# Optimization experiments

Measured on AMD Instinct MI355X. Metric: run time of the kernel, lower is better.

Reference implementation:

```python
import jax, jax.numpy as jnp
import numpy as np
from jax import lax

BOS = 1


def setup_inputs() -> dict:
    key = jax.random.key(0)
    ks = jax.random.split(key, 12)
    B, T_ENC, D_ENC = 32, 800, 512   # D_ENC == att_odim
    E, H, V, ATT_H = 256, 512, 10000, 512
    s = 0.02
    return {
        "enc_pad": jax.random.normal(ks[0], (B, T_ENC, D_ENC), jnp.float32),
        "embedding": jax.random.normal(ks[1], (V, E), jnp.float32) * s,
        "W_ih": jax.random.normal(ks[2], (4 * H, E + D_ENC), jnp.float32) * s,
        "W_hh": jax.random.normal(ks[3], (4 * H, H), jnp.float32) * s,
        "b_ih": jnp.zeros((4 * H,), jnp.float32),
        "b_hh": jnp.zeros((4 * H,), jnp.float32),
        "W_enc": jax.random.normal(ks[4], (D_ENC, ATT_H), jnp.float32) * s,
        "W_dec": jax.random.normal(ks[5], (H, ATT_H), jnp.float32) * s,
        "v_att": jax.random.normal(ks[6], (ATT_H,), jnp.float32) * s,
        "W_out": jax.random.normal(ks[7], (V, H + D_ENC), jnp.float32) * s,
        "b_out": jnp.zeros((V,), jnp.float32),
        "enc_len": jax.random.randint(ks[8], (B,), 1, T_ENC + 1).astype(jnp.int32),
        "max_dec_timesteps": 100,
    }


def reference(enc_pad, embedding, W_ih, W_hh, b_ih, b_hh,
              W_enc, W_dec, v_att, W_out, b_out,
              enc_len, max_dec_timesteps):
    B, T, D = enc_pad.shape
    H = W_hh.shape[1]
    mask = jnp.arange(T)[None, :] < enc_len[:, None]          # [B,T]
    enc_proj = jnp.einsum('btd,da->bta', enc_pad, W_enc)       # precomputed enc keys
    NEG = jnp.float32(-1e30)

    def step(carry, _):
        dec_z, dec_c, c, pred = carry
        emb = jnp.take(embedding, pred, axis=0)                # [B,E]
        x = jnp.concatenate([emb, c], axis=-1)                 # cell_inp
        # torch.nn.LSTMCell gates
        gates = x @ W_ih.T + b_ih + dec_z @ W_hh.T + b_hh
        i, f, g, o = jnp.split(gates, 4, axis=-1)
        i, f, o = jax.nn.sigmoid(i), jax.nn.sigmoid(f), jax.nn.sigmoid(o)
        g = jnp.tanh(g)
        dec_c = f * dec_c + i * g
        dec_z = o * jnp.tanh(dec_c)
        # additive attention over encoder frames, masked by enc_len
        e = jnp.tanh(enc_proj + (dec_z @ W_dec)[:, None, :]) @ v_att  # [B,T]
        w = jax.nn.softmax(jnp.where(mask, e, NEG), axis=-1)
        c = jnp.einsum('bt,btd->bd', w, enc_pad)               # context, dim att_odim
        logit = jnp.concatenate([dec_z, c], axis=-1) @ W_out.T + b_out
        pred = jnp.argmax(logit, axis=-1)
        return (dec_z, dec_c, c, pred), (logit, pred, w)

    init = (jnp.zeros((B, H), enc_pad.dtype),
            jnp.zeros((B, H), enc_pad.dtype),
            jnp.zeros((B, D), enc_pad.dtype),
            jnp.full((B,), BOS, jnp.int32))
    _, (logits, preds, ws) = lax.scan(step, init, None, length=int(max_dec_timesteps))
    logits = jnp.swapaxes(logits, 0, 1)                        # [B,Tdec,V]
    preds = jnp.swapaxes(preds, 0, 1)                          # [B,Tdec]
    ws = jnp.swapaxes(ws, 0, 1)                                # [B,Tdec,Tenc]
    log_probs = jax.nn.log_softmax(logits, axis=2)
    ys_log_probs = jnp.take_along_axis(log_probs, preds[..., None], axis=2)[..., 0]
    return ys_log_probs, preds, ws
```

## Files before the change

### kernel.cpp

```cpp
#include <hip/hip_runtime.h>
#include <math.h>

#define B 32
#define T 800
#define E 256
#define H 512
#define V 10000
#define S 100

typedef float f4 __attribute__((ext_vector_type(4)));

#define OFF_ENCP 0
#define OFF_GP   (OFF_ENCP + B*T*512)
#define OFF_ZB   (OFF_GP + 4*B*2048)
#define OFF_DECC (OFF_ZB + B*512)
#define OFF_QV   (OFF_DECC + 2*B*512)
#define OFF_PB   (OFF_QV + B*512)
#define OFF_PSL  (OFF_PB + B*T)
#define OFF_CP   (OFF_PSL + B*16)
#define OFF_CTX  (OFF_CP + B*16*512)
#define OFF_KEY  (OFF_CTX + B*512)
#define OFF_ESUM (OFF_KEY + 128)

__device__ __forceinline__ float tanh_fast(float x) {
    float e = __expf(2.0f * x);
    return 1.0f - __fdividef(2.0f, e + 1.0f);
}

__global__ __launch_bounds__(256) void k_encproj(const float* Ap, const float* Wenc, float* outp) {
    __shared__ float Ast[16][68];
    __shared__ float Bs[16][68];
    int rb = blockIdx.x, cb = blockIdx.y;
    int tid = threadIdx.x;
    int tx = tid & 15, ty = tid >> 4;
    float acc[4][4] = {};
    for (int kb = 0; kb < 32; kb++) {
        #pragma unroll
        for (int i = 0; i < 4; i++) {
            int idx = tid + i*256;
            int r = idx >> 4, k = idx & 15;
            Ast[k][r] = Ap[(rb*64 + r)*512 + kb*16 + k];
        }
        #pragma unroll
        for (int i = 0; i < 4; i++) {
            int idx = tid + i*256;
            int k = idx >> 6, c = idx & 63;
            Bs[k][c] = Wenc[(kb*16 + k)*512 + cb*64 + c];
        }
        __syncthreads();
        #pragma unroll
        for (int kk = 0; kk < 16; kk++) {
            f4 a4 = *(const f4*)&Ast[kk][ty*4];
            f4 b4 = *(const f4*)&Bs[kk][tx*4];
            #pragma unroll
            for (int i = 0; i < 4; i++)
                #pragma unroll
                for (int j = 0; j < 4; j++)
                    acc[i][j] += a4[i] * b4[j];
        }
        __syncthreads();
    }
    #pragma unroll
    for (int i = 0; i < 4; i++)
        #pragma unroll
        for (int j = 0; j < 4; j++)
            outp[(rb*64 + ty*4 + i)*512 + cb*64 + tx*4 + j] = acc[i][j];
}

__global__ __launch_bounds__(512) void k_init(float* ws) {
    int idx = blockIdx.x*512 + threadIdx.x;
    ws[OFF_ZB + idx] = 0.f;
    ws[OFF_CTX + idx] = 0.f;
    ws[OFF_DECC + B*512 + idx] = 0.f;
    if (blockIdx.x == 0 && threadIdx.x < 32) {
        unsigned long long* key = (unsigned long long*)(ws + OFF_KEY);
        key[32 + threadIdx.x] = 0xFFFFFFFEull;
    }
}

__global__ __launch_bounds__(512) void ka_gates(const float* __restrict__ Wih,
    const float* __restrict__ Whh, const float* __restrict__ emb,
    float* __restrict__ ws, float* __restrict__ outp, int s) {
    __shared__ float xs[32*324];
    __shared__ float wt[32*324];
    __shared__ float part[8*32*33];
    __shared__ int preds[32];
    const int tid = threadIdx.x;
    const int jt = blockIdx.x, kq = blockIdx.y;
    const int p = s & 1;
    unsigned long long* keys = (unsigned long long*)(ws + OFF_KEY);
    float* esum = ws + OFF_ESUM;
    if (tid < 32) {
        unsigned long long k = keys[(p^1)*32 + tid];
        int pr = (int)(0xFFFFFFFFu - (unsigned)(k & 0xFFFFFFFFull));
        preds[tid] = pr;
        if (jt == 0 && kq == 0) {
            if (s > 0) {
                unsigned mu = (unsigned)(k >> 32);
                unsigned ou = (mu & 0x80000000u) ? (mu & 0x7FFFFFFFu) : ~mu;
                outp[tid*S + (s-1)] = __uint_as_float(ou) - logf(esum[(p^1)*32 + tid]);
                outp[B*S + tid*S + (s-1)] = (float)pr;
            }
            keys[p*32 + tid] = 0ull;
            esum[p*32 + tid] = 0.f;
        }
    }
    __syncthreads();
    const float* cbuf = ws + OFF_CTX;
    const float* zbuf = ws + OFF_ZB;
    #pragma unroll
    for (int i = 0; i < 5; i++) {
        int idx = tid + i*512;
        int b = idx / 80, c4 = idx - b*80;
        int k = kq*320 + c4*4;
        f4 v;
        if (k < 256)      v = *(const f4*)&emb[(size_t)preds[b]*E + k];
        else if (k < 768) v = *(const f4*)&cbuf[b*512 + (k-256)];
        else              v = *(const f4*)&zbuf[b*512 + (k-768)];
        *(f4*)&xs[b*324 + c4*4] = v;
    }
    #pragma unroll
    for (int i = 0; i < 5; i++) {
        int idx = tid + i*512;
        int r = idx / 80, c4 = idx - r*80;
        int kk = kq*320 + c4*4;
        int j = jt*32 + r;
        f4 v = (kk < 768) ? *(const f4*)&Wih[(size_t)j*768 + kk]
                          : *(const f4*)&Whh[(size_t)j*512 + (kk - 768)];
        *(f4*)&wt[r*324 + c4*4] = v;
    }
    __syncthreads();
    const int wid = tid >> 6, l = tid & 63;
    const int j0 = (l >> 3)*4, b0 = (l & 7)*4;
    const int ks0 = wid*40;
    float acc[4][4] = {};
    #pragma unroll 2
    for (int it = 0; it < 10; it++) {
        int k = ks0 + it*4;
        f4 w[4], x[4];
        #pragma unroll
        for (int i = 0; i < 4; i++) w[i] = *(const f4*)&wt[(j0 + i)*324 + k];
        #pragma unroll
        for (int j = 0; j < 4; j++) x[j] = *(const f4*)&xs[(b0 + j)*324 + k];
        #pragma unroll
        for (int i = 0; i < 4; i++)
            #pragma unroll
            for (int j = 0; j < 4; j++)
                acc[i][j] += w[i][0]*x[j][0] + w[i][1]*x[j][1]
                           + w[i][2]*x[j][2] + w[i][3]*x[j][3];
    }
    __syncthreads();
    #pragma unroll
    for (int i = 0; i < 4; i++)
        #pragma unroll
        for (int j = 0; j < 4; j++)
            part[wid*1056 + (j0 + i)*33 + (b0 + j)] = acc[i][j];
    __syncthreads();
    #pragma unroll
    for (int u = 0; u < 2; u++) {
        int o = tid + u*512;
        int j = o >> 5, b = o & 31;
        float g = 0.f;
        #pragma unroll
        for (int w2 = 0; w2 < 8; w2++) g += part[w2*1056 + j*33 + b];
        ws[OFF_GP + (kq*32 + b)*2048 + jt*32 + j] = g;
    }
}

__global__ __launch_bounds__(512) void kq_lstmq(const float* __restrict__ Wdec,
    const float* __restrict__ bih, const float* __restrict__ bhh,
    float* __restrict__ ws, int s) {
    __shared__ float zs[516];
    __shared__ float pq[32*68];
    const int tid = threadIdx.x;
    const int b = blockIdx.x, as = blockIdx.y;
    const int p = s & 1;
    const float* dold = ws + OFF_DECC + (p^1)*B*512;
    float* dnew = ws + OFF_DECC + p*B*512;
    {
        int h = tid;
        float gv[4];
        #pragma unroll
        for (int g = 0; g < 4; g++) {
            float sacc = bih[g*512 + h] + bhh[g*512 + h];
            #pragma unroll
            for (int kc = 0; kc < 4; kc++)
                sacc += ws[OFF_GP + (kc*32 + b)*2048 + g*512 + h];
            gv[g] = sacc;
        }
        float ig = 1.f/(1.f + expf(-gv[0]));
        float fg = 1.f/(1.f + expf(-gv[1]));
        float g2 = tanhf(gv[2]);
        float og = 1.f/(1.f + expf(-gv[3]));
        float c = fg*dold[b*512 + h] + ig*g2;
        float z = og*tanhf(c);
        zs[h] = z;
        if (as == 0) {
            dnew[b*512 + h] = c;
            ws[OFF_ZB + b*512 + h] = z;
        }
    }
    __syncthreads();
    {
        const int aq = tid & 15, ks = tid >> 4;
        const int a0 = as*64 + aq*4;
        f4 accq = {0.f, 0.f, 0.f, 0.f};
        #pragma unroll
        for (int kk = 0; kk < 16; kk += 4) {
            int k = ks*16 + kk;
            f4 z4 = *(const f4*)&zs[k];
            f4 w0 = *(const f4*)&Wdec[(size_t)(k+0)*512 + a0];
            f4 w1 = *(const f4*)&Wdec[(size_t)(k+1)*512 + a0];
            f4 w2 = *(const f4*)&Wdec[(size_t)(k+2)*512 + a0];
            f4 w3 = *(const f4*)&Wdec[(size_t)(k+3)*512 + a0];
            accq += z4[0]*w0 + z4[1]*w1 + z4[2]*w2 + z4[3]*w3;
        }
        *(f4*)&pq[ks*68 + aq*4] = accq;
    }
    __syncthreads();
    if (tid < 64) {
        float q = 0.f;
        #pragma unroll
        for (int ks = 0; ks < 32; ks++) q += pq[ks*68 + tid];
        ws[OFF_QV + b*512 + as*64 + tid] = q;
    }
}

__global__ __launch_bounds__(512) void kb_ectx(const float* __restrict__ encpad,
    const float* __restrict__ vatt, const int* __restrict__ enclen,
    float* __restrict__ ws) {
    __shared__ float qs[512];
    __shared__ float vs[512];
    __shared__ float ep[50*132];
    __shared__ float p8[64][9];
    __shared__ float pl[52];
    const int tid = threadIdx.x;
    const int b = blockIdx.x >> 4, ts = blockIdx.x & 15;
    const int len = enclen[b];
    const int t0 = ts*50;
    const int nt = min(t0 + 50, len) - t0;
    qs[tid] = ws[OFF_QV + b*512 + tid];
    vs[tid] = vatt[tid];
    if (tid < 52) pl[tid] = 0.f;
    if (tid < 50) ws[OFF_PB + b*800 + t0 + tid] = 0.f;
    __syncthreads();
    const int c4 = tid & 127, tg = tid >> 7;
    const f4 q4 = *(const f4*)&qs[c4*4];
    const f4 vv = *(const f4*)&vs[c4*4];
    #pragma unroll
    for (int k = 0; k < 13; k++) {
        int tt = tg + 4*k;
        if (tt < nt) {
            f4 e4 = *(const f4*)&ws[OFF_ENCP + ((size_t)(b*800 + t0 + tt))*512 + c4*4];
            float sv = tanh_fast(e4[0]+q4[0])*vv[0] + tanh_fast(e4[1]+q4[1])*vv[1]
                     + tanh_fast(e4[2]+q4[2])*vv[2] + tanh_fast(e4[3]+q4[3])*vv[3];
            ep[tt*132 + c4] = sv;
        }
    }
    __syncthreads();
    {
        int t = tid >> 3, j = tid & 7;
        if (t < nt) {
            float sv = 0.f;
            #pragma unroll
            for (int m = 0; m < 16; m++) sv += ep[t*132 + j*16 + m];
            p8[t][j] = sv;
        }
    }
    __syncthreads();
    if (tid < nt) {
        float e = 0.f;
        #pragma unroll
        for (int j = 0; j < 8; j++) e += p8[tid][j];
        float pv = __expf(e);
        pl[tid] = pv;
        ws[OFF_PB + b*800 + t0 + tid] = pv;
    }
    __syncthreads();
    if (tid == 0) {
        float sacc = 0.f;
        for (int i = 0; i < 50; i++) sacc += pl[i];
        ws[OFF_PSL + b*16 + ts] = sacc;
    }
    f4 acc = {0.f, 0.f, 0.f, 0.f};
    #pragma unroll
    for (int k = 0; k < 13; k++) {
        int tt = tg + 4*k;
        if (tt < nt) {
            f4 e4 = *(const f4*)&encpad[((size_t)(b*800 + t0 + tt))*512 + c4*4];
            acc += pl[tt]*e4;
        }
    }
    __syncthreads();
    *(f4*)&ep[(tg*128 + c4)*4] = acc;
    __syncthreads();
    if (tid < 128) {
        f4 c = {0.f, 0.f, 0.f, 0.f};
        #pragma unroll
        for (int g = 0; g < 4; g++) c += *(const f4*)&ep[(g*128 + tid)*4];
        *(f4*)&ws[OFF_CP + (size_t)(b*16 + ts)*512 + tid*4] = c;
    }
}

__global__ __launch_bounds__(512) void kr_ctx(float* __restrict__ ws,
    float* __restrict__ outp, int s) {
    const int tid = threadIdx.x, b = blockIdx.x;
    __shared__ float invs;
    if (tid == 0) {
        float sacc = 0.f;
        #pragma unroll
        for (int i = 0; i < 16; i++) sacc += ws[OFF_PSL + b*16 + i];
        invs = 1.f / sacc;
    }
    __syncthreads();
    float inv = invs;
    {
        float c = 0.f;
        #pragma unroll
        for (int t2 = 0; t2 < 16; t2++) c += ws[OFF_CP + (size_t)(b*16 + t2)*512 + tid];
        ws[OFF_CTX + b*512 + tid] = c * inv;
    }
    float* wrow = outp + 2*B*S + (size_t)(b*S + s)*T;
    for (int t = tid; t < 800; t += 512)
        wrow[t] = ws[OFF_PB + b*800 + t] * inv;
}

__global__ __launch_bounds__(512) void kc_logits(const float* __restrict__ Wout,
    const float* __restrict__ bout, float* __restrict__ ws, int s) {
    __shared__ float sm[32*1028];
    const int tid = threadIdx.x, blk = blockIdx.x;
    const int p = s & 1;
    const int v0 = blk*40;
    #pragma unroll
    for (int i = 0; i < 8; i++) {
        int o = tid + i*512;
        int bb = o >> 7, qq = o & 127;
        *(f4*)&sm[bb*1028 + qq*4] = *(const f4*)&ws[OFF_ZB + bb*512 + qq*4];
        *(f4*)&sm[bb*1028 + 512 + qq*4] = *(const f4*)&ws[OFF_CTX + bb*512 + qq*4];
    }
    __syncthreads();
    const int wid = tid >> 6, l = tid & 63;
    const int vq = l & 7, bq2 = l >> 3;
    float acc[5][4] = {};
    const int kb = wid*128;
    const float* wbase = &Wout[(size_t)(v0 + vq*5)*1024 + kb];
    #pragma unroll 2
    for (int g = 0; g < 32; g++) {
        f4 w[5];
        #pragma unroll
        for (int i = 0; i < 5; i++) w[i] = *(const f4*)&wbase[i*1024 + g*4];
        #pragma unroll
        for (int j = 0; j < 4; j++) {
            f4 x4 = *(const f4*)&sm[(bq2+8*j)*1028 + kb + g*4];
            #pragma unroll
            for (int i = 0; i < 5; i++)
                acc[i][j] += w[i][0]*x4[0] + w[i][1]*x4[1] + w[i][2]*x4[2] + w[i][3]*x4[3];
        }
    }
    __syncthreads();
    #pragma unroll
    for (int i = 0; i < 5; i++)
        #pragma unroll
        for (int j = 0; j < 4; j++)
            sm[wid*1320 + (vq*5+i)*33 + (bq2+8*j)] = acc[i][j];
    __syncthreads();
    if (tid < 256) {
        int b = tid >> 3, u = tid & 7;
        float bmax = -3.0e38f; int bidx = 0; float bsum = 0.f;
        #pragma unroll
        for (int i = 0; i < 5; i++) {
            int r = u*5 + i;
            float lv = bout[v0 + r];
            #pragma unroll
            for (int w2 = 0; w2 < 8; w2++) lv += sm[w2*1320 + r*33 + b];
            bsum += __expf(lv);
            if (lv > bmax) { bmax = lv; bidx = v0 + r; }
        }
        #pragma unroll
        for (int off = 1; off < 8; off <<= 1) {
            float ov = __shfl_xor(bmax, off, 64);
            int oi = __shfl_xor(bidx, off, 64);
            float os = __shfl_xor(bsum, off, 64);
            bsum += os;
            if (ov > bmax || (ov == bmax && oi < bidx)) { bmax = ov; bidx = oi; }
        }
        if (u == 0) {
            unsigned mu = __float_as_uint(bmax);
            mu = (mu & 0x80000000u) ? ~mu : (mu | 0x80000000u);
            unsigned long long kk = ((unsigned long long)mu << 32)
                                  | (unsigned long long)(0xFFFFFFFFu - (unsigned)bidx);
            atomicMax((unsigned long long*)(ws + OFF_KEY) + p*32 + b, kk);
            atomicAdd(ws + OFF_ESUM + p*32 + b, bsum);
        }
    }
}

__global__ __launch_bounds__(64) void k_final(float* __restrict__ ws, float* __restrict__ outp) {
    int b = threadIdx.x;
    if (b < 32) {
        unsigned long long k = ((unsigned long long*)(ws + OFF_KEY))[32 + b];
        unsigned mu = (unsigned)(k >> 32);
        unsigned ou = (mu & 0x80000000u) ? (mu & 0x7FFFFFFFu) : ~mu;
        int pr = (int)(0xFFFFFFFFu - (unsigned)(k & 0xFFFFFFFFull));
        outp[b*S + 99] = __uint_as_float(ou) - logf(ws[OFF_ESUM + 32 + b]);
        outp[B*S + b*S + 99] = (float)pr;
    }
}

extern "C" void kernel_launch(void* const* d_in, const int* in_sizes, int n_in,
                              void* d_out, int out_size, void* d_ws, size_t ws_size,
                              hipStream_t stream) {
    (void)in_sizes; (void)n_in; (void)out_size; (void)ws_size;
    const float* encpad = (const float*)d_in[0];
    const float* emb    = (const float*)d_in[1];
    const float* Wih    = (const float*)d_in[2];
    const float* Whh    = (const float*)d_in[3];
    const float* bih    = (const float*)d_in[4];
    const float* bhh    = (const float*)d_in[5];
    const float* Wenc   = (const float*)d_in[6];
    const float* Wdec   = (const float*)d_in[7];
    const float* vatt   = (const float*)d_in[8];
    const float* Wout   = (const float*)d_in[9];
    const float* bout   = (const float*)d_in[10];
    const int*   enclen = (const int*)d_in[11];
    float* outp = (float*)d_out;
    float* ws   = (float*)d_ws;

    k_init<<<32, 512, 0, stream>>>(ws);
    k_encproj<<<dim3(400, 8), 256, 0, stream>>>(encpad, Wenc, ws + OFF_ENCP);

    for (int s = 0; s < S; s++) {
        ka_gates<<<dim3(64, 4), 512, 0, stream>>>(Wih, Whh, emb, ws, outp, s);
        kq_lstmq<<<dim3(32, 8), 512, 0, stream>>>(Wdec, bih, bhh, ws, s);
        kb_ectx<<<512, 512, 0, stream>>>(encpad, vatt, enclen, ws);
        kr_ctx<<<32, 512, 0, stream>>>(ws, outp, s);
        kc_logits<<<250, 512, 0, stream>>>(Wout, bout, ws, s);
    }
    k_final<<<1, 64, 0, stream>>>(ws, outp);
}
```

Baseline: 7.917 ms.

## Split output projection, overlap decoder-state half with attention kernel

The logits GEMM is split into a dec_z half and a context half. The dec_z half (plus bias) now runs in extra blocks of the attention/context kernel and writes partial logits to a padded workspace buffer. The context-only half then runs after the context reduction. The reduction kernel is also spread over 4x more blocks. This takes half of the output-projection work off the serial critical path, at the cost of writing and re-reading partial logits and running 4 of 8 warps idle in the logit blocks.

```diff
diff --git a/kernel.cpp b/kernel.cpp
--- a/kernel.cpp
+++ b/kernel.cpp
@@ -7,6 +7,7 @@
 #define H 512
 #define V 10000
 #define S 100
+#define VP 10016
 
 typedef float f4 __attribute__((ext_vector_type(4)));
 
@@ -21,6 +22,7 @@
 #define OFF_CTX  (OFF_CP + B*16*512)
 #define OFF_KEY  (OFF_CTX + B*512)
 #define OFF_ESUM (OFF_KEY + 128)
+#define OFF_LP   (OFF_ESUM + 64)
 
 __device__ __forceinline__ float tanh_fast(float x) {
     float e = __expf(2.0f * x);
@@ -226,85 +228,139 @@
     }
 }
 
-__global__ __launch_bounds__(512) void kb_ectx(const float* __restrict__ encpad,
+__global__ __launch_bounds__(512) void kbz(const float* __restrict__ encpad,
     const float* __restrict__ vatt, const int* __restrict__ enclen,
+    const float* __restrict__ Wout, const float* __restrict__ bout,
     float* __restrict__ ws) {
-    __shared__ float qs[512];
-    __shared__ float vs[512];
-    __shared__ float ep[50*132];
-    __shared__ float p8[64][9];
-    __shared__ float pl[52];
-    const int tid = threadIdx.x;
-    const int b = blockIdx.x >> 4, ts = blockIdx.x & 15;
-    const int len = enclen[b];
-    const int t0 = ts*50;
-    const int nt = min(t0 + 50, len) - t0;
-    qs[tid] = ws[OFF_QV + b*512 + tid];
-    vs[tid] = vatt[tid];
-    if (tid < 52) pl[tid] = 0.f;
-    if (tid < 50) ws[OFF_PB + b*800 + t0 + tid] = 0.f;
-    __syncthreads();
-    const int c4 = tid & 127, tg = tid >> 7;
-    const f4 q4 = *(const f4*)&qs[c4*4];
-    const f4 vv = *(const f4*)&vs[c4*4];
-    #pragma unroll
-    for (int k = 0; k < 13; k++) {
-        int tt = tg + 4*k;
-        if (tt < nt) {
-            f4 e4 = *(const f4*)&ws[OFF_ENCP + ((size_t)(b*800 + t0 + tt))*512 + c4*4];
-            float sv = tanh_fast(e4[0]+q4[0])*vv[0] + tanh_fast(e4[1]+q4[1])*vv[1]
-                     + tanh_fast(e4[2]+q4[2])*vv[2] + tanh_fast(e4[3]+q4[3])*vv[3];
-            ep[tt*132 + c4] = sv;
-        }
-    }
-    __syncthreads();
-    {
-        int t = tid >> 3, j = tid & 7;
-        if (t < nt) {
-            float sv = 0.f;
-            #pragma unroll
-            for (int m = 0; m < 16; m++) sv += ep[t*132 + j*16 + m];
-            p8[t][j] = sv;
-        }
-    }
-    __syncthreads();
-    if (tid < nt) {
-        float e = 0.f;
-        #pragma unroll
-        for (int j = 0; j < 8; j++) e += p8[tid][j];
-        float pv = __expf(e);
-        pl[tid] = pv;
-        ws[OFF_PB + b*800 + t0 + tid] = pv;
-    }
-    __syncthreads();
-    if (tid == 0) {
-        float sacc = 0.f;
-        for (int i = 0; i < 50; i++) sacc += pl[i];
-        ws[OFF_PSL + b*16 + ts] = sacc;
-    }
-    f4 acc = {0.f, 0.f, 0.f, 0.f};
-    #pragma unroll
-    for (int k = 0; k < 13; k++) {
-        int tt = tg + 4*k;
-        if (tt < nt) {
-            f4 e4 = *(const f4*)&encpad[((size_t)(b*800 + t0 + tt))*512 + c4*4];
-            acc += pl[tt]*e4;
-        }
-    }
-    __syncthreads();
-    *(f4*)&ep[(tg*128 + c4)*4] = acc;
-    __syncthreads();
-    if (tid < 128) {
-        f4 c = {0.f, 0.f, 0.f, 0.f};
-        #pragma unroll
-        for (int g = 0; g < 4; g++) c += *(const f4*)&ep[(g*128 + tid)*4];
-        *(f4*)&ws[OFF_CP + (size_t)(b*16 + ts)*512 + tid*4] = c;
+    __shared__ float sm[16512];
+    const int tid = threadIdx.x, blk = blockIdx.x;
+    if (blk < 512) {
+        float* qs = sm;
+        float* vs = sm + 512;
+        float* ep = sm + 1024;
+        float* p8 = sm + 7624;
+        float* pl = sm + 8200;
+        const int b = blk >> 4, ts = blk & 15;
+        const int len = enclen[b];
+        const int t0 = ts*50;
+        const int nt = min(t0 + 50, len) - t0;
+        qs[tid] = ws[OFF_QV + b*512 + tid];
+        vs[tid] = vatt[tid];
+        if (tid < 52) pl[tid] = 0.f;
+        if (tid < 50) ws[OFF_PB + b*800 + t0 + tid] = 0.f;
+        __syncthreads();
+        const int c4 = tid & 127, tg = tid >> 7;
+        const f4 q4 = *(const f4*)&qs[c4*4];
+        const f4 vv = *(const f4*)&vs[c4*4];
+        #pragma unroll
+        for (int k = 0; k < 13; k++) {
+            int tt = tg + 4*k;
+            if (tt < nt) {
+                f4 e4 = *(const f4*)&ws[OFF_ENCP + ((size_t)(b*800 + t0 + tt))*512 + c4*4];
+                float sv = tanh_fast(e4[0]+q4[0])*vv[0] + tanh_fast(e4[1]+q4[1])*vv[1]
+                         + tanh_fast(e4[2]+q4[2])*vv[2] + tanh_fast(e4[3]+q4[3])*vv[3];
+                ep[tt*132 + c4] = sv;
+            }
+        }
+        __syncthreads();
+        {
+            int t = tid >> 3, j = tid & 7;
+            if (t < nt) {
+                float sv = 0.f;
+                #pragma unroll
+                for (int m = 0; m < 16; m++) sv += ep[t*132 + j*16 + m];
+                p8[t*9 + j] = sv;
+            }
+        }
+        __syncthreads();
+        if (tid < nt) {
+            float e = 0.f;
+            #pragma unroll
+            for (int j = 0; j < 8; j++) e += p8[tid*9 + j];
+            float pv = __expf(e);
+            pl[tid] = pv;
+            ws[OFF_PB + b*800 + t0 + tid] = pv;
+        }
+        __syncthreads();
+        if (tid == 0) {
+            float sacc = 0.f;
+            for (int i = 0; i < 50; i++) sacc += pl[i];
+            ws[OFF_PSL + b*16 + ts] = sacc;
+        }
+        f4 acc = {0.f, 0.f, 0.f, 0.f};
+        #pragma unroll
+        for (int k = 0; k < 13; k++) {
+            int tt = tg + 4*k;
+            if (tt < nt) {
+                f4 e4 = *(const f4*)&encpad[((size_t)(b*800 + t0 + tt))*512 + c4*4];
+                acc += pl[tt]*e4;
+            }
+        }
+        __syncthreads();
+        *(f4*)&ep[(tg*128 + c4)*4] = acc;
+        __syncthreads();
+        if (tid < 128) {
+            f4 c = {0.f, 0.f, 0.f, 0.f};
+            #pragma unroll
+            for (int g = 0; g < 4; g++) c += *(const f4*)&ep[(g*128 + tid)*4];
+            *(f4*)&ws[OFF_CP + (size_t)(b*16 + ts)*512 + tid*4] = c;
+        }
+    } else {
+        const int v0 = (blk - 512)*40;
+        #pragma unroll
+        for (int i = 0; i < 8; i++) {
+            int o = tid + i*512;
+            int bb = o >> 7, qq = o & 127;
+            *(f4*)&sm[bb*516 + qq*4] = *(const f4*)&ws[OFF_ZB + bb*512 + qq*4];
+        }
+        __syncthreads();
+        const int wid = tid >> 6, l = tid & 63;
+        const int vq = l & 7, bq2 = l >> 3;
+        float acc[5][4] = {};
+        if (wid < 4) {
+            const int kb = wid*128;
+            const float* wbase = &Wout[(size_t)(v0 + vq*5)*1024 + kb];
+            #pragma unroll 2
+            for (int g = 0; g < 32; g++) {
+                f4 w[5];
+                #pragma unroll
+                for (int i = 0; i < 5; i++) w[i] = *(const f4*)&wbase[i*1024 + g*4];
+                #pragma unroll
+                for (int j = 0; j < 4; j++) {
+                    f4 x4 = *(const f4*)&sm[(bq2+8*j)*516 + kb + g*4];
+                    #pragma unroll
+                    for (int i = 0; i < 5; i++)
+                        acc[i][j] += w[i][0]*x4[0] + w[i][1]*x4[1]
+                                   + w[i][2]*x4[2] + w[i][3]*x4[3];
+                }
+            }
+        }
+        __syncthreads();
+        if (wid < 4) {
+            #pragma unroll
+            for (int i = 0; i < 5; i++)
+                #pragma unroll
+                for (int j = 0; j < 4; j++)
+                    sm[wid*1320 + (vq*5+i)*33 + (bq2+8*j)] = acc[i][j];
+        }
+        __syncthreads();
+        if (tid < 256) {
+            int b = tid >> 3, u = tid & 7;
+            #pragma unroll
+            for (int i = 0; i < 5; i++) {
+                int r = u*5 + i;
+                float lv = bout[v0 + r];
+                #pragma unroll
+                for (int w2 = 0; w2 < 4; w2++) lv += sm[w2*1320 + r*33 + b];
+                ws[OFF_LP + b*VP + v0 + r] = lv;
+            }
+        }
     }
 }
 
 __global__ __launch_bounds__(512) void kr_ctx(float* __restrict__ ws,
     float* __restrict__ outp, int s) {
-    const int tid = threadIdx.x, b = blockIdx.x;
+    const int tid = threadIdx.x, b = blockIdx.x, dsl = blockIdx.y;
     __shared__ float invs;
     if (tid == 0) {
         float sacc = 0.f;
@@ -314,20 +370,22 @@
     }
     __syncthreads();
     float inv = invs;
-    {
+    if (tid < 128) {
+        int d = dsl*128 + tid;
         float c = 0.f;
         #pragma unroll
-        for (int t2 = 0; t2 < 16; t2++) c += ws[OFF_CP + (size_t)(b*16 + t2)*512 + tid];
-        ws[OFF_CTX + b*512 + tid] = c * inv;
-    }
-    float* wrow = outp + 2*B*S + (size_t)(b*S + s)*T;
-    for (int t = tid; t < 800; t += 512)
-        wrow[t] = ws[OFF_PB + b*800 + t] * inv;
-}
-
-__global__ __launch_bounds__(512) void kc_logits(const float* __restrict__ Wout,
-    const float* __restrict__ bout, float* __restrict__ ws, int s) {
-    __shared__ float sm[32*1028];
+        for (int t2 = 0; t2 < 16; t2++) c += ws[OFF_CP + (size_t)(b*16 + t2)*512 + d];
+        ws[OFF_CTX + b*512 + d] = c * inv;
+    }
+    if (tid < 200) {
+        int t = dsl*200 + tid;
+        outp[2*B*S + (size_t)(b*S + s)*T + t] = ws[OFF_PB + b*800 + t] * inv;
+    }
+}
+
+__global__ __launch_bounds__(512) void kc2_logits(const float* __restrict__ Wout,
+    float* __restrict__ ws, int s) {
+    __shared__ float sm[16512];
     const int tid = threadIdx.x, blk = blockIdx.x;
     const int p = s & 1;
     const int v0 = blk*40;
@@ -335,34 +393,38 @@
     for (int i = 0; i < 8; i++) {
         int o = tid + i*512;
         int bb = o >> 7, qq = o & 127;
-        *(f4*)&sm[bb*1028 + qq*4] = *(const f4*)&ws[OFF_ZB + bb*512 + qq*4];
-        *(f4*)&sm[bb*1028 + 512 + qq*4] = *(const f4*)&ws[OFF_CTX + bb*512 + qq*4];
+        *(f4*)&sm[bb*516 + qq*4] = *(const f4*)&ws[OFF_CTX + bb*512 + qq*4];
     }
     __syncthreads();
     const int wid = tid >> 6, l = tid & 63;
     const int vq = l & 7, bq2 = l >> 3;
     float acc[5][4] = {};
-    const int kb = wid*128;
-    const float* wbase = &Wout[(size_t)(v0 + vq*5)*1024 + kb];
-    #pragma unroll 2
-    for (int g = 0; g < 32; g++) {
-        f4 w[5];
-        #pragma unroll
-        for (int i = 0; i < 5; i++) w[i] = *(const f4*)&wbase[i*1024 + g*4];
-        #pragma unroll
-        for (int j = 0; j < 4; j++) {
-            f4 x4 = *(const f4*)&sm[(bq2+8*j)*1028 + kb + g*4];
-            #pragma unroll
-            for (int i = 0; i < 5; i++)
-                acc[i][j] += w[i][0]*x4[0] + w[i][1]*x4[1] + w[i][2]*x4[2] + w[i][3]*x4[3];
-        }
-    }
-    __syncthreads();
-    #pragma unroll
-    for (int i = 0; i < 5; i++)
-        #pragma unroll
-        for (int j = 0; j < 4; j++)
-            sm[wid*1320 + (vq*5+i)*33 + (bq2+8*j)] = acc[i][j];
+    if (wid < 4) {
+        const int kb = wid*128;
+        const float* wbase = &Wout[(size_t)(v0 + vq*5)*1024 + 512 + kb];
+        #pragma unroll 2
+        for (int g = 0; g < 32; g++) {
+            f4 w[5];
+            #pragma unroll
+            for (int i = 0; i < 5; i++) w[i] = *(const f4*)&wbase[i*1024 + g*4];
+            #pragma unroll
+            for (int j = 0; j < 4; j++) {
+                f4 x4 = *(const f4*)&sm[(bq2+8*j)*516 + kb + g*4];
+                #pragma unroll
+                for (int i = 0; i < 5; i++)
+                    acc[i][j] += w[i][0]*x4[0] + w[i][1]*x4[1]
+                               + w[i][2]*x4[2] + w[i][3]*x4[3];
+            }
+        }
+    }
+    __syncthreads();
+    if (wid < 4) {
+        #pragma unroll
+        for (int i = 0; i < 5; i++)
+            #pragma unroll
+            for (int j = 0; j < 4; j++)
+                sm[wid*1320 + (vq*5+i)*33 + (bq2+8*j)] = acc[i][j];
+    }
     __syncthreads();
     if (tid < 256) {
         int b = tid >> 3, u = tid & 7;
@@ -370,9 +432,9 @@
         #pragma unroll
         for (int i = 0; i < 5; i++) {
             int r = u*5 + i;
-            float lv = bout[v0 + r];
-            #pragma unroll
-            for (int w2 = 0; w2 < 8; w2++) lv += sm[w2*1320 + r*33 + b];
+            float lv = ws[OFF_LP + b*VP + v0 + r];
+            #pragma unroll
+            for (int w2 = 0; w2 < 4; w2++) lv += sm[w2*1320 + r*33 + b];
             bsum += __expf(lv);
             if (lv > bmax) { bmax = lv; bidx = v0 + r; }
         }
@@ -432,9 +494,9 @@
     for (int s = 0; s < S; s++) {
         ka_gates<<<dim3(64, 4), 512, 0, stream>>>(Wih, Whh, emb, ws, outp, s);
         kq_lstmq<<<dim3(32, 8), 512, 0, stream>>>(Wdec, bih, bhh, ws, s);
-        kb_ectx<<<512, 512, 0, stream>>>(encpad, vatt, enclen, ws);
-        kr_ctx<<<32, 512, 0, stream>>>(ws, outp, s);
-        kc_logits<<<250, 512, 0, stream>>>(Wout, bout, ws, s);
+        kbz<<<762, 512, 0, stream>>>(encpad, vatt, enclen, Wout, bout, ws);
+        kr_ctx<<<dim3(32, 4), 512, 0, stream>>>(ws, outp, s);
+        kc2_logits<<<250, 512, 0, stream>>>(Wout, ws, s);
     }
     k_final<<<1, 64, 0, stream>>>(ws, outp);
 }
```

Result: slower. 9.493 ms (+19.9%).
